# Kernel tuning notes

Hardware: AMD Instinct MI355X
Metric: run time of the kernel (lower is better)

The kernel has to match this reference:

```python
import jax, jax.numpy as jnp
import numpy as np

S = 3072      # total tokens across all images
DIM = 1280    # hidden_size
H = 16        # num_heads
HD = DIM // H # head_dim = 80
NSEG = 6      # number of images (cu_seqlens has NSEG+1 entries)


def _rotate_half(x):
    x1, x2 = jnp.split(x, 2, axis=-1)
    return jnp.concatenate([-x2, x1], axis=-1)


def setup_inputs() -> dict:
    key = jax.random.key(0)
    ks = jax.random.split(key, 12)
    hidden_states = jax.random.normal(ks[0], (S, DIM), jnp.float32)
    # realistic vision rotary embedding: half-dim inv_freq, repeated to head_dim
    inv_freq = 1.0 / (10000.0 ** (jnp.arange(0, HD // 2, dtype=jnp.float32) / (HD // 2)))
    freqs = jnp.arange(S, dtype=jnp.float32)[:, None] * inv_freq[None, :]  # [S, HD/2]
    emb = jnp.concatenate([freqs, freqs], axis=-1)  # [S, HD]
    cos = jnp.cos(emb)
    sin = jnp.sin(emb)
    sc = 0.02
    wq = jax.random.normal(ks[1], (DIM, DIM), jnp.float32) * sc
    bq = jax.random.normal(ks[2], (DIM,), jnp.float32) * sc
    wk = jax.random.normal(ks[3], (DIM, DIM), jnp.float32) * sc
    bk = jax.random.normal(ks[4], (DIM,), jnp.float32) * sc
    wv = jax.random.normal(ks[5], (DIM, DIM), jnp.float32) * sc
    bv = jax.random.normal(ks[6], (DIM,), jnp.float32) * sc
    wo = jax.random.normal(ks[7], (DIM, DIM), jnp.float32) * sc
    bo = jax.random.normal(ks[8], (DIM,), jnp.float32) * sc
    cu_seqlens = (jnp.arange(NSEG + 1, dtype=jnp.int32) * (S // NSEG))  # [0,512,...,3072]
    return dict(hidden_states=hidden_states, cos=cos, sin=sin,
                wq=wq, bq=bq, wk=wk, bk=bk, wv=wv, bv=bv, wo=wo, bo=bo,
                cu_seqlens=cu_seqlens)


def reference(hidden_states, cos, sin, wq, bq, wk, bk, wv, bv, wo, bo, cu_seqlens):
    seq_length = hidden_states.shape[0]
    scaling = HD ** (-0.5)
    # QKV projections (torch Linear: x @ W.T + b)
    q = (hidden_states @ wq.T + bq).reshape(seq_length, H, HD)
    k = (hidden_states @ wk.T + bk).reshape(seq_length, H, HD)
    v = (hidden_states @ wv.T + bv).reshape(seq_length, H, HD)
    # apply_rotary_pos_emb_vision: cos/sin [S, HD] broadcast over head axis
    c = cos[:, None, :]
    s = sin[:, None, :]
    q = q * c + _rotate_half(q) * s
    k = k * c + _rotate_half(k) * s
    # block-diagonal (per-image) attention via segment mask
    seg = jnp.searchsorted(cu_seqlens[1:], jnp.arange(seq_length), side='right')
    mask = seg[:, None] == seg[None, :]  # [S, S] bool
    scores = jnp.einsum('shd,thd->hst', q, k) * scaling  # [H, S, S]
    scores = jnp.where(mask[None, :, :], scores, jnp.finfo(scores.dtype).min)
    attn = jax.nn.softmax(scores, axis=-1)
    out = jnp.einsum('hst,thd->shd', attn, v).reshape(seq_length, DIM)
    return out @ wo.T + bo
```

## Files before the change

kernel.cpp:

```cpp
#include <hip/hip_runtime.h>
#include <hip/hip_bf16.h>
#include <hip/hip_fp16.h>
#include <cstdint>
#include <cstddef>

typedef _Float16 f16;
typedef f16 f16x2 __attribute__((ext_vector_type(2)));
typedef f16 f16x4 __attribute__((ext_vector_type(4)));
typedef f16 f16x8 __attribute__((ext_vector_type(8)));
typedef float f32x4 __attribute__((ext_vector_type(4)));

#define S_LEN 3072
#define DIM 1280
#define NH 16
#define HD 80
#define SEG 512

#define MFMA16F(a, b, c) __builtin_amdgcn_mfma_f32_16x16x32_f16((a), (b), (c), 0, 0, 0)

__device__ __forceinline__ void gl2lds16(const void* g, void* l) {
    __builtin_amdgcn_global_load_lds(
        (const __attribute__((address_space(1))) unsigned int*)g,
        (__attribute__((address_space(3))) unsigned int*)l, 16, 0, 0);
}

__device__ __forceinline__ unsigned int pack2(float a, float b) {
    f16x2 t = {(f16)a, (f16)b};
    union { f16x2 v; unsigned int u; } c;
    c.v = t;
    return c.u;
}

__global__ __launch_bounds__(256) void cvt_kernel(
    const float* __restrict__ hs,
    const float* __restrict__ wq, const float* __restrict__ wk,
    const float* __restrict__ wv, const float* __restrict__ wo,
    f16* __restrict__ hs16,
    f16* __restrict__ wq16, f16* __restrict__ wk16,
    f16* __restrict__ wv16, f16* __restrict__ wo16)
{
    const int m = blockIdx.y;
    const float* src; f16* dst; int n4;
    if (m == 0)      { src = hs; dst = hs16; n4 = S_LEN * DIM / 4; }
    else if (m == 1) { src = wq; dst = wq16; n4 = DIM * DIM / 4; }
    else if (m == 2) { src = wk; dst = wk16; n4 = DIM * DIM / 4; }
    else if (m == 3) { src = wv; dst = wv16; n4 = DIM * DIM / 4; }
    else             { src = wo; dst = wo16; n4 = DIM * DIM / 4; }
    int idx = blockIdx.x * 256 + threadIdx.x;
    if (idx >= n4) return;
    f32x4 v = *(const f32x4*)(src + (size_t)idx * 4);
    f16x4 o;
#pragma unroll
    for (int e = 0; e < 4; ++e) o[e] = (f16)v[e];
    *(f16x4*)(dst + (size_t)idx * 4) = o;
}

__global__ __launch_bounds__(256) void gemm_f16_kernel(
    const f16* __restrict__ A,
    const f16* __restrict__ W0, const f16* __restrict__ W1, const f16* __restrict__ W2,
    const float* __restrict__ b0, const float* __restrict__ b1, const float* __restrict__ b2,
    f16* __restrict__ O0, f16* __restrict__ O1, f16* __restrict__ vT)
{
    const int f = blockIdx.x;
    const int xcd = f & 7;
    const int idx = f >> 3;
    const int mt = xcd * 3 + idx % 3;
    const int yz = idx / 3;
    const int nt = yz % 10;
    const int mode = yz / 10;

    const f16* W = (mode == 1) ? W1 : (mode == 2) ? W2 : W0;
    const float* bias = (mode == 1) ? b1 : (mode == 2) ? b2 : b0;

    __shared__ __align__(16) f16 As[128 * 32];
    __shared__ __align__(16) f16 Bs[128 * 32];

    const int tid = threadIdx.x;
    const int lane = tid & 63;
    const int lane15 = tid & 15;
    const int quad = lane >> 4;
    const int w = tid >> 6;
    const int wm = (w >> 1) * 64;
    const int wn = (w & 1) * 64;
    const int m0 = mt * 128;
    const int n0 = nt * 128;

    const int srow = w * 32 + (lane >> 2);
    const int scol = (lane & 3) * 8;
    const f16* gA0 = A + (size_t)(m0 + srow) * DIM + scol;
    const f16* gA1 = A + (size_t)(m0 + srow + 16) * DIM + scol;
    const f16* gB0 = W + (size_t)(n0 + srow) * DIM + scol;
    const f16* gB1 = W + (size_t)(n0 + srow + 16) * DIM + scol;
    f16* lA0 = As + (w * 32) * 32;
    f16* lA1 = As + (w * 32 + 16) * 32;
    f16* lB0 = Bs + (w * 32) * 32;
    f16* lB1 = Bs + (w * 32 + 16) * 32;

    f32x4 acc[4][4];
#pragma unroll
    for (int i = 0; i < 4; ++i)
#pragma unroll
        for (int j = 0; j < 4; ++j)
            acc[i][j] = (f32x4){0.f, 0.f, 0.f, 0.f};

    for (int kt = 0; kt < DIM / 32; ++kt) {
        __syncthreads();
        gl2lds16(gA0 + kt * 32, lA0);
        gl2lds16(gA1 + kt * 32, lA1);
        gl2lds16(gB0 + kt * 32, lB0);
        gl2lds16(gB1 + kt * 32, lB1);
        __syncthreads();

        f16x8 fa[4], fb[4];
#pragma unroll
        for (int i = 0; i < 4; ++i)
            fa[i] = *(const f16x8*)(As + (wm + i * 16 + lane15) * 32 + quad * 8);
#pragma unroll
        for (int j = 0; j < 4; ++j)
            fb[j] = *(const f16x8*)(Bs + (wn + j * 16 + lane15) * 32 + quad * 8);
#pragma unroll
        for (int i = 0; i < 4; ++i)
#pragma unroll
            for (int j = 0; j < 4; ++j)
                acc[i][j] = MFMA16F(fa[i], fb[j], acc[i][j]);
    }

    float bvv[4];
#pragma unroll
    for (int j = 0; j < 4; ++j)
        bvv[j] = bias[n0 + wn + j * 16 + lane15];

    if (mode == 2) {
#pragma unroll
        for (int i = 0; i < 4; ++i)
#pragma unroll
            for (int j = 0; j < 4; ++j) {
                f16x4 ov;
#pragma unroll
                for (int r = 0; r < 4; ++r) ov[r] = (f16)(acc[i][j][r] + bvv[j]);
                int row = m0 + wm + i * 16 + quad * 4;
                int col = n0 + wn + j * 16 + lane15;
                *(f16x4*)(vT + (size_t)col * S_LEN + row) = ov;
            }
    } else {
        f16* O = (mode == 0) ? O0 : O1;
#pragma unroll
        for (int i = 0; i < 4; ++i)
#pragma unroll
            for (int j = 0; j < 4; ++j)
#pragma unroll
                for (int r = 0; r < 4; ++r) {
                    int row = m0 + wm + i * 16 + quad * 4 + r;
                    int col = n0 + wn + j * 16 + lane15;
                    O[(size_t)row * DIM + col] = (f16)(acc[i][j][r] + bvv[j]);
                }
    }
}

__global__ __launch_bounds__(256) void gemm_out_kernel(
    const f16* __restrict__ A, const f16* __restrict__ W,
    const float* __restrict__ bias, float* __restrict__ OF)
{
    const int f = blockIdx.x;
    const int xcd = f & 7;
    const int idx = f >> 3;
    const int xt = xcd * 6 + idx % 6;
    const int yt = idx / 6;

    __shared__ __align__(16) f16 As[64 * 32];
    __shared__ __align__(16) f16 Bs[128 * 32];

    const int tid = threadIdx.x;
    const int lane = tid & 63;
    const int lane15 = tid & 15;
    const int quad = lane >> 4;
    const int w = tid >> 6;
    const int wn = w * 32;
    const int m0 = xt * 64;
    const int n0 = yt * 128;

    const int srA = w * 16 + (lane >> 2);
    const int srB = w * 32 + (lane >> 2);
    const int scol = (lane & 3) * 8;
    const f16* gA0 = A + (size_t)(m0 + srA) * DIM + scol;
    const f16* gB0 = W + (size_t)(n0 + srB) * DIM + scol;
    const f16* gB1 = W + (size_t)(n0 + srB + 16) * DIM + scol;
    f16* lA0 = As + (w * 16) * 32;
    f16* lB0 = Bs + (w * 32) * 32;
    f16* lB1 = Bs + (w * 32 + 16) * 32;

    f32x4 acc[4][2];
#pragma unroll
    for (int i = 0; i < 4; ++i)
#pragma unroll
        for (int j = 0; j < 2; ++j)
            acc[i][j] = (f32x4){0.f, 0.f, 0.f, 0.f};

    for (int kt = 0; kt < DIM / 32; ++kt) {
        __syncthreads();
        gl2lds16(gA0 + kt * 32, lA0);
        gl2lds16(gB0 + kt * 32, lB0);
        gl2lds16(gB1 + kt * 32, lB1);
        __syncthreads();

        f16x8 fa[4], fb[2];
#pragma unroll
        for (int i = 0; i < 4; ++i)
            fa[i] = *(const f16x8*)(As + (i * 16 + lane15) * 32 + quad * 8);
#pragma unroll
        for (int j = 0; j < 2; ++j)
            fb[j] = *(const f16x8*)(Bs + (wn + j * 16 + lane15) * 32 + quad * 8);
#pragma unroll
        for (int i = 0; i < 4; ++i)
#pragma unroll
            for (int j = 0; j < 2; ++j)
                acc[i][j] = MFMA16F(fa[i], fb[j], acc[i][j]);
    }

    float bvv[2];
#pragma unroll
    for (int j = 0; j < 2; ++j)
        bvv[j] = bias[n0 + wn + j * 16 + lane15];

#pragma unroll
    for (int i = 0; i < 4; ++i)
#pragma unroll
        for (int j = 0; j < 2; ++j)
#pragma unroll
            for (int r = 0; r < 4; ++r) {
                int row = m0 + i * 16 + quad * 4 + r;
                int col = n0 + wn + j * 16 + lane15;
                OF[(size_t)row * DIM + col] = acc[i][j][r] + bvv[j];
            }
}

__global__ __launch_bounds__(256) void rope_kernel(
    f16* __restrict__ qb, f16* __restrict__ kb,
    const float* __restrict__ cosb, const float* __restrict__ sinb)
{
    int idx = blockIdx.x * 256 + threadIdx.x;
    int c = idx % 5;
    int t = idx / 5;
    int h = t & 15; t >>= 4;
    int s = t % S_LEN;
    int which = t / S_LEN;
    f16* buf = which ? kb : qb;
    float scale = which ? 1.0f : 0.11180339887498948f;
    int j = c * 8;
    f32x4 ca = *(const f32x4*)(cosb + s * HD + j);
    f32x4 cb = *(const f32x4*)(cosb + s * HD + j + 4);
    f32x4 sna = *(const f32x4*)(sinb + s * HD + j);
    f32x4 snb = *(const f32x4*)(sinb + s * HD + j + 4);
    size_t base = (size_t)s * DIM + h * HD + j;
    f16x8 x1 = *(f16x8*)(buf + base);
    f16x8 x2 = *(f16x8*)(buf + base + 40);
    f16x8 o1, o2;
#pragma unroll
    for (int e = 0; e < 8; ++e) {
        float ce = (e < 4) ? ca[e] : cb[e - 4];
        float se = (e < 4) ? sna[e] : snb[e - 4];
        float a = (float)x1[e], b = (float)x2[e];
        o1[e] = (f16)((a * ce - b * se) * scale);
        o2[e] = (f16)((b * ce + a * se) * scale);
    }
    *(f16x8*)(buf + base) = o1;
    *(f16x8*)(buf + base + 40) = o2;
}

__global__ __launch_bounds__(256) void attn_kernel(
    const f16* __restrict__ q, const f16* __restrict__ k,
    const f16* __restrict__ vT, f16* __restrict__ o)
{
    const int h = blockIdx.x;
    const int g = blockIdx.y;
    const int qc = blockIdx.z;
    const int tid = threadIdx.x;
    const int lane15 = tid & 15;
    const int quad = (tid & 63) >> 4;
    const int w = tid >> 6;
    const int qbase = g * SEG + qc * 64;
    const int qrow = qbase + w * 16 + lane15;

    __shared__ __align__(16) f16 Ks[128 * 88];
    __shared__ __align__(16) f16 Vt[80 * 128];

    f16x8 zf;
#pragma unroll
    for (int e = 0; e < 8; ++e) zf[e] = (f16)0.0f;

    f16x8 fq[3];
#pragma unroll
    for (int kc = 0; kc < 3; ++kc) {
        if (kc == 2 && quad >= 2) fq[kc] = zf;
        else fq[kc] = *(const f16x8*)(q + (size_t)qrow * DIM + h * HD + kc * 32 + quad * 8);
    }

    float m_run = -1e30f, l_run = 0.f;
    f32x4 Oa[5];
#pragma unroll
    for (int dt = 0; dt < 5; ++dt) Oa[dt] = (f32x4){0.f, 0.f, 0.f, 0.f};

    for (int kt = 0; kt < 4; ++kt) {
        __syncthreads();
        const int kb = g * SEG + kt * 128;
#pragma unroll
        for (int c = tid; c < 1280; c += 256) {
            int r = c / 10;
            int c8 = (c - r * 10) * 8;
            *(f16x8*)(Ks + r * 88 + c8) =
                *(const f16x8*)(k + (size_t)(kb + r) * DIM + h * HD + c8);
        }
#pragma unroll
        for (int c = tid; c < 1280; c += 256) {
            int d = c >> 4;
            int sc = c & 15;
            *(f16x8*)(Vt + d * 128 + (sc ^ (d & 7)) * 8) =
                *(const f16x8*)(vT + (size_t)(h * HD + d) * S_LEN + kb + sc * 8);
        }
        __syncthreads();

        f32x4 sa[8];
#pragma unroll
        for (int nt = 0; nt < 8; ++nt) sa[nt] = (f32x4){0.f, 0.f, 0.f, 0.f};
#pragma unroll
        for (int kc = 0; kc < 3; ++kc) {
#pragma unroll
            for (int nt = 0; nt < 8; ++nt) {
                f16x8 fk;
                if (kc == 2 && quad >= 2) fk = zf;
                else fk = *(const f16x8*)(Ks + (nt * 16 + lane15) * 88 + kc * 32 + quad * 8);
                sa[nt] = MFMA16F(fk, fq[kc], sa[nt]);
            }
        }

        float mt = -1e30f;
#pragma unroll
        for (int nt = 0; nt < 8; ++nt)
#pragma unroll
            for (int r = 0; r < 4; ++r) mt = fmaxf(mt, sa[nt][r]);
        mt = fmaxf(mt, __shfl_xor(mt, 16, 64));
        mt = fmaxf(mt, __shfl_xor(mt, 32, 64));

        float mn = fmaxf(m_run, mt);
        float alpha = __expf(m_run - mn);
        m_run = mn;
        float lt = 0.f;
        unsigned int pp[8][2];
#pragma unroll
        for (int nt = 0; nt < 8; ++nt) {
            float p0 = __expf(sa[nt][0] - mn);
            float p1 = __expf(sa[nt][1] - mn);
            float p2 = __expf(sa[nt][2] - mn);
            float p3 = __expf(sa[nt][3] - mn);
            lt += (p0 + p1) + (p2 + p3);
            pp[nt][0] = pack2(p0, p1);
            pp[nt][1] = pack2(p2, p3);
        }
        lt += __shfl_xor(lt, 16, 64);
        lt += __shfl_xor(lt, 32, 64);
        l_run = l_run * alpha + lt;

#pragma unroll
        for (int dt = 0; dt < 5; ++dt)
#pragma unroll
            for (int r = 0; r < 4; ++r) Oa[dt][r] *= alpha;

        const int srcA = ((quad & 1) * 2) * 16 + lane15;
        const int srcB = srcA + 16;
        const bool hi = quad >= 2;
#pragma unroll
        for (int kc2 = 0; kc2 < 4; ++kc2) {
            unsigned int e0 = __shfl((int)pp[2 * kc2][0], srcA, 64);
            unsigned int e1 = __shfl((int)pp[2 * kc2][1], srcA, 64);
            unsigned int e2 = __shfl((int)pp[2 * kc2][0], srcB, 64);
            unsigned int e3 = __shfl((int)pp[2 * kc2][1], srcB, 64);
            unsigned int o0 = __shfl((int)pp[2 * kc2 + 1][0], srcA, 64);
            unsigned int o1 = __shfl((int)pp[2 * kc2 + 1][1], srcA, 64);
            unsigned int o2 = __shfl((int)pp[2 * kc2 + 1][0], srcB, 64);
            unsigned int o3 = __shfl((int)pp[2 * kc2 + 1][1], srcB, 64);
            union { unsigned int u[4]; f16x8 v; } fp;
            fp.u[0] = hi ? o0 : e0;
            fp.u[1] = hi ? o1 : e1;
            fp.u[2] = hi ? o2 : e2;
            fp.u[3] = hi ? o3 : e3;
#pragma unroll
            for (int dt = 0; dt < 5; ++dt) {
                int drow = dt * 16 + lane15;
                int slot = (kc2 * 4 + quad) ^ (drow & 7);
                f16x8 fv = *(const f16x8*)(Vt + drow * 128 + slot * 8);
                Oa[dt] = MFMA16F(fv, fp.v, Oa[dt]);
            }
        }
    }

    float inv = 1.0f / l_run;
#pragma unroll
    for (int dt = 0; dt < 5; ++dt) {
        f16x4 ov;
#pragma unroll
        for (int r = 0; r < 4; ++r) ov[r] = (f16)(Oa[dt][r] * inv);
        *(f16x4*)(o + (size_t)qrow * DIM + h * HD + dt * 16 + quad * 4) = ov;
    }
}

extern "C" void kernel_launch(void* const* d_in, const int* in_sizes, int n_in,
                              void* d_out, int out_size, void* d_ws, size_t ws_size,
                              hipStream_t stream)
{
    const float* hs   = (const float*)d_in[0];
    const float* cosb = (const float*)d_in[1];
    const float* sinb = (const float*)d_in[2];
    const float* wq   = (const float*)d_in[3];
    const float* bq   = (const float*)d_in[4];
    const float* wk   = (const float*)d_in[5];
    const float* bk   = (const float*)d_in[6];
    const float* wv   = (const float*)d_in[7];
    const float* bv   = (const float*)d_in[8];
    const float* wo   = (const float*)d_in[9];
    const float* bo   = (const float*)d_in[10];

    const size_t SD = (size_t)S_LEN * DIM;
    const size_t WW = (size_t)DIM * DIM;
    f16* hs16 = (f16*)d_ws;
    f16* wq16 = hs16 + SD;
    f16* wk16 = wq16 + WW;
    f16* wv16 = wk16 + WW;
    f16* wo16 = wv16 + WW;
    f16* q16  = wo16 + WW;
    f16* k16  = q16 + SD;
    f16* vT16 = k16 + SD;
    f16* ao16 = vT16 + SD;
    float* outb = (float*)d_out;

    cvt_kernel<<<dim3(S_LEN * DIM / 4 / 256, 5), 256, 0, stream>>>(
        hs, wq, wk, wv, wo, hs16, wq16, wk16, wv16, wo16);
    gemm_f16_kernel<<<720, 256, 0, stream>>>(
        hs16, wq16, wk16, wv16, bq, bk, bv, q16, k16, vT16);
    rope_kernel<<<1920, 256, 0, stream>>>(q16, k16, cosb, sinb);
    attn_kernel<<<dim3(NH, 6, 8), 256, 0, stream>>>(q16, k16, vT16, ao16);
    gemm_out_kernel<<<480, 256, 0, stream>>>(ao16, wo16, bo, outb);
}
```

Baseline: 217.7 us.

## Load GEMM operand fragments directly from global memory, dropping LDS staging

Both the QKV projection GEMM and the output projection GEMM now have each wave load its MFMA A/B fragments straight from global memory into registers. This replaces the cooperative global-to-LDS copy and its two barriers per k-step, and the loop is unrolled by two so loads can overlap. The aim is to remove synchronization and LDS round-trip latency. The cost is redundant global/L2 traffic, since waves sharing rows or columns each fetch them separately, and the accesses are strided, less coalesced 16-byte loads.

```diff
diff --git a/kernel.cpp b/kernel.cpp
--- a/kernel.cpp
+++ b/kernel.cpp
@@ -17,12 +17,6 @@
 #define SEG 512
 
 #define MFMA16F(a, b, c) __builtin_amdgcn_mfma_f32_16x16x32_f16((a), (b), (c), 0, 0, 0)
-
-__device__ __forceinline__ void gl2lds16(const void* g, void* l) {
-    __builtin_amdgcn_global_load_lds(
-        (const __attribute__((address_space(1))) unsigned int*)g,
-        (__attribute__((address_space(3))) unsigned int*)l, 16, 0, 0);
-}
 
 __device__ __forceinline__ unsigned int pack2(float a, float b) {
     f16x2 t = {(f16)a, (f16)b};
@@ -62,18 +56,14 @@
     f16* __restrict__ O0, f16* __restrict__ O1, f16* __restrict__ vT)
 {
     const int f = blockIdx.x;
-    const int xcd = f & 7;
     const int idx = f >> 3;
-    const int mt = xcd * 3 + idx % 3;
+    const int mt = (f & 7) * 3 + idx % 3;
     const int yz = idx / 3;
     const int nt = yz % 10;
     const int mode = yz / 10;
 
     const f16* W = (mode == 1) ? W1 : (mode == 2) ? W2 : W0;
     const float* bias = (mode == 1) ? b1 : (mode == 2) ? b2 : b0;
-
-    __shared__ __align__(16) f16 As[128 * 32];
-    __shared__ __align__(16) f16 Bs[128 * 32];
 
     const int tid = threadIdx.x;
     const int lane = tid & 63;
@@ -85,16 +75,14 @@
     const int m0 = mt * 128;
     const int n0 = nt * 128;
 
-    const int srow = w * 32 + (lane >> 2);
-    const int scol = (lane & 3) * 8;
-    const f16* gA0 = A + (size_t)(m0 + srow) * DIM + scol;
-    const f16* gA1 = A + (size_t)(m0 + srow + 16) * DIM + scol;
-    const f16* gB0 = W + (size_t)(n0 + srow) * DIM + scol;
-    const f16* gB1 = W + (size_t)(n0 + srow + 16) * DIM + scol;
-    f16* lA0 = As + (w * 32) * 32;
-    f16* lA1 = As + (w * 32 + 16) * 32;
-    f16* lB0 = Bs + (w * 32) * 32;
-    f16* lB1 = Bs + (w * 32 + 16) * 32;
+    const f16* pa[4];
+    const f16* pb[4];
+#pragma unroll
+    for (int i = 0; i < 4; ++i)
+        pa[i] = A + (size_t)(m0 + wm + i * 16 + lane15) * DIM + quad * 8;
+#pragma unroll
+    for (int j = 0; j < 4; ++j)
+        pb[j] = W + (size_t)(n0 + wn + j * 16 + lane15) * DIM + quad * 8;
 
     f32x4 acc[4][4];
 #pragma unroll
@@ -103,21 +91,13 @@
         for (int j = 0; j < 4; ++j)
             acc[i][j] = (f32x4){0.f, 0.f, 0.f, 0.f};
 
+#pragma unroll 2
     for (int kt = 0; kt < DIM / 32; ++kt) {
-        __syncthreads();
-        gl2lds16(gA0 + kt * 32, lA0);
-        gl2lds16(gA1 + kt * 32, lA1);
-        gl2lds16(gB0 + kt * 32, lB0);
-        gl2lds16(gB1 + kt * 32, lB1);
-        __syncthreads();
-
         f16x8 fa[4], fb[4];
 #pragma unroll
-        for (int i = 0; i < 4; ++i)
-            fa[i] = *(const f16x8*)(As + (wm + i * 16 + lane15) * 32 + quad * 8);
-#pragma unroll
-        for (int j = 0; j < 4; ++j)
-            fb[j] = *(const f16x8*)(Bs + (wn + j * 16 + lane15) * 32 + quad * 8);
+        for (int i = 0; i < 4; ++i) fa[i] = *(const f16x8*)(pa[i] + kt * 32);
+#pragma unroll
+        for (int j = 0; j < 4; ++j) fb[j] = *(const f16x8*)(pb[j] + kt * 32);
 #pragma unroll
         for (int i = 0; i < 4; ++i)
 #pragma unroll
@@ -162,13 +142,9 @@
     const float* __restrict__ bias, float* __restrict__ OF)
 {
     const int f = blockIdx.x;
-    const int xcd = f & 7;
     const int idx = f >> 3;
-    const int xt = xcd * 6 + idx % 6;
+    const int xt = (f & 7) * 6 + idx % 6;
     const int yt = idx / 6;
-
-    __shared__ __align__(16) f16 As[64 * 32];
-    __shared__ __align__(16) f16 Bs[128 * 32];
 
     const int tid = threadIdx.x;
     const int lane = tid & 63;
@@ -179,15 +155,14 @@
     const int m0 = xt * 64;
     const int n0 = yt * 128;
 
-    const int srA = w * 16 + (lane >> 2);
-    const int srB = w * 32 + (lane >> 2);
-    const int scol = (lane & 3) * 8;
-    const f16* gA0 = A + (size_t)(m0 + srA) * DIM + scol;
-    const f16* gB0 = W + (size_t)(n0 + srB) * DIM + scol;
-    const f16* gB1 = W + (size_t)(n0 + srB + 16) * DIM + scol;
-    f16* lA0 = As + (w * 16) * 32;
-    f16* lB0 = Bs + (w * 32) * 32;
-    f16* lB1 = Bs + (w * 32 + 16) * 32;
+    const f16* pa[4];
+    const f16* pb[2];
+#pragma unroll
+    for (int i = 0; i < 4; ++i)
+        pa[i] = A + (size_t)(m0 + i * 16 + lane15) * DIM + quad * 8;
+#pragma unroll
+    for (int j = 0; j < 2; ++j)
+        pb[j] = W + (size_t)(n0 + wn + j * 16 + lane15) * DIM + quad * 8;
 
     f32x4 acc[4][2];
 #pragma unroll
@@ -196,20 +171,13 @@
         for (int j = 0; j < 2; ++j)
             acc[i][j] = (f32x4){0.f, 0.f, 0.f, 0.f};
 
+#pragma unroll 2
     for (int kt = 0; kt < DIM / 32; ++kt) {
-        __syncthreads();
-        gl2lds16(gA0 + kt * 32, lA0);
-        gl2lds16(gB0 + kt * 32, lB0);
-        gl2lds16(gB1 + kt * 32, lB1);
-        __syncthreads();
-
         f16x8 fa[4], fb[2];
 #pragma unroll
-        for (int i = 0; i < 4; ++i)
-            fa[i] = *(const f16x8*)(As + (i * 16 + lane15) * 32 + quad * 8);
-#pragma unroll
-        for (int j = 0; j < 2; ++j)
-            fb[j] = *(const f16x8*)(Bs + (wn + j * 16 + lane15) * 32 + quad * 8);
+        for (int i = 0; i < 4; ++i) fa[i] = *(const f16x8*)(pa[i] + kt * 32);
+#pragma unroll
+        for (int j = 0; j < 2; ++j) fb[j] = *(const f16x8*)(pb[j] + kt * 32);
 #pragma unroll
         for (int i = 0; i < 4; ++i)
 #pragma unroll
```

Result: slower. 326.7 us (+50.1%).
